# Kernel tuning notes

Measured on AMD Instinct MI355X. Metric: run time of the kernel, lower is better.

The kernel has to match this reference:

```python
import jax, jax.numpy as jnp
import numpy as np

BETA = 0.25


def setup_inputs() -> dict:
    key = jax.random.key(0)
    k1, k2 = jax.random.split(key)
    z = jax.random.normal(k1, (16, 2048, 256), dtype=jnp.float32)
    # n_q=4 codebooks, each [n_e=2048, e_dim=256]; xavier-ish scale
    W = jax.random.normal(k2, (4, 2048, 256), dtype=jnp.float32) * 0.05
    return {"z": z, "W": W}


def reference(z, W):
    """Residual VQ forward (p=1.0, eval-mode math). Returns (z_q, loss, indices)."""
    n_q, n_e, e_dim = W.shape
    lead = z.shape[:-1]
    flat_shape = (-1, e_dim)

    residual = z
    cumulative_q = jnp.zeros_like(z)
    losses = []
    idx_list = []
    for k in range(n_q):
        Wk = W[k]  # [n_e, e_dim]
        flat = residual.reshape(flat_shape)  # [N, e_dim]
        dist = (
            jnp.sum(flat * flat, axis=1, keepdims=True)
            - 2.0 * (flat @ Wk.T)
            + jnp.sum(Wk * Wk, axis=1)[None, :]
        )
        idx = jnp.argmin(dist, axis=1)  # [N]
        # one_hot @ Wk is mathematically a gather of codebook rows
        q = Wk[idx].reshape(residual.shape)
        # commit + beta*codebook; both are (residual.detach() - q)^2.mean(-1)
        diff = jax.lax.stop_gradient(residual) - q
        losses.append((1.0 + BETA) * jnp.mean(diff * diff, axis=-1))
        cumulative_q = cumulative_q + q
        residual = residual - q
        idx_list.append(idx.reshape(*lead, 1))

    # straight-through: gradient of z_q flows only to z
    z_q = z + jax.lax.stop_gradient(cumulative_q - z)
    total_loss = jnp.mean(jnp.stack(losses, axis=0).mean(axis=0))
    indices = jnp.concatenate(idx_list, axis=-1)  # [..., n_q]
    return z_q, total_loss, indices
```

## Files before the change

kernel.cpp:

```cpp
#include <hip/hip_runtime.h>
#include <cstdint>
#include <math.h>
#include <float.h>

#define N_Q   4
#define NROWS 32768
#define EDIM  256
#define NE    2048
#define NCT_H 64
#define TM    32
#define NTHREADS 256

#define ZQ_SIZE  (NROWS * EDIM)
#define LOSS_OFF ZQ_SIZE
#define IDX_OFF  (ZQ_SIZE + 1)

#define TAU 0.012f

typedef __attribute__((ext_vector_type(8))) _Float16 f16x8;
typedef __attribute__((ext_vector_type(4))) float    f32x4;

union F8 { _Float16 h[8]; f16x8 v; };

__device__ __forceinline__ float np_block128_sq(const float* __restrict__ p) {
    #pragma clang fp contract(off)
    float r[8];
    #pragma unroll
    for (int j = 0; j < 8; ++j) { float v = p[j]; r[j] = v * v; }
    for (int i = 8; i < 128; i += 8) {
        #pragma unroll
        for (int j = 0; j < 8; ++j) { float v = p[i + j]; float sq = v * v; r[j] = r[j] + sq; }
    }
    return ((r[0] + r[1]) + (r[2] + r[3])) + ((r[4] + r[5]) + (r[6] + r[7]));
}

__global__ __launch_bounds__(256) void wsq_kernel(const float* __restrict__ W,
                                                  float* __restrict__ wsq32) {
    __shared__ float rowbuf[4][EDIM];
    int wv   = threadIdx.x >> 6;
    int row  = blockIdx.x * 4 + (threadIdx.x >> 6);
    int lane = threadIdx.x & 63;
    float4 v = ((const float4*)(W + (size_t)row * EDIM))[lane];
    *(float4*)&rowbuf[wv][lane * 4] = v;
    __syncthreads();
    if (lane == 0) {
        float a = np_block128_sq(rowbuf[wv]);
        float b = np_block128_sq(rowbuf[wv] + 128);
        wsq32[row] = a + b;
    }
}

__global__ __launch_bounds__(256) void wh_kernel(const float* __restrict__ W,
                                                 short* __restrict__ wh) {
    int gid  = blockIdx.x * 256 + threadIdx.x;
    int lane = gid & 63;
    int grp  = gid >> 6;
    int ctq  = grp >> 3;
    int ks   = grp & 7;
    int n = lane & 15, kq = lane >> 4;
    const float* src = W + (((size_t)(ctq * 16 + n)) << 8) + ks * 32 + kq * 8;
    float4 p0 = *(const float4*)src;
    float4 p1 = *(const float4*)(src + 4);
    float v[8] = {p0.x, p0.y, p0.z, p0.w, p1.x, p1.y, p1.z, p1.w};
    F8 h;
    #pragma unroll
    for (int j = 0; j < 8; ++j) h.h[j] = (_Float16)v[j];
    *(f16x8*)(wh + (((size_t)grp) << 9) + lane * 8) = h.v;
}

__device__ __forceinline__ void top3_merge(float& a1, int& ai1, float& a2, int& ai2, float& a3,
                                           float b1, int bi1, float b2, int bi2, float b3) {
    float c1, c2, c3; int k1, k2;
    if (b1 < a1 || (b1 == a1 && bi1 < ai1)) {
        c1 = b1; k1 = bi1;
        if (a1 < b2 || (a1 == b2 && ai1 < bi2)) { c2 = a1; k2 = ai1; c3 = fminf(b2, a2); }
        else                                    { c2 = b2; k2 = bi2; c3 = fminf(a1, b3); }
    } else {
        c1 = a1; k1 = ai1;
        if (b1 < a2 || (b1 == a2 && bi1 < ai2)) { c2 = b1; k2 = bi1; c3 = fminf(a2, b2); }
        else                                    { c2 = a2; k2 = ai2; c3 = fminf(b1, a3); }
    }
    a1 = c1; ai1 = k1; a2 = c2; ai2 = k2; a3 = c3;
}

__global__ __launch_bounds__(256, 4) void rvq_main(
    const float* __restrict__ z, const float* __restrict__ W,
    const float* __restrict__ wsq32, const short* __restrict__ wh,
    float* __restrict__ resd_g, float* __restrict__ out,
    float* __restrict__ loss_partial)
{
    __shared__ __align__(16) short lds_b[2][2][4][512];
    __shared__ float Srow[TM];
    __shared__ float rm1[2][TM], rm2[2][TM], rm3[2][TM];
    __shared__ int   ri1[2][TM], ri2[2][TM];
    __shared__ int   idx_s[TM], is2_s[TM];
    __shared__ int   rk_cnt, rk_list[TM];
    __shared__ int   pr_cnt, pr_list[TM];
    __shared__ float rrow_s[EDIM];
    __shared__ float red_f[NTHREADS];
    __shared__ int   red_i[NTHREADS];
    __shared__ float wavesum[4];

    const int tid  = threadIdx.x;
    const int wave = tid >> 6;
    const int lane = tid & 63;
    const int n    = lane & 15;
    const int kq   = lane >> 4;
    const int half = wave >> 1;
    const int rsel = wave & 1;
    const int row0 = blockIdx.x * TM;
    const int rowg = row0 + rsel * 16;

    for (int i = tid; i < TM * 64; i += NTHREADS) {
        int r = i >> 6, c = i & 63;
        ((float4*)resd_g)[(((size_t)(row0 + r)) << 6) + c] =
            ((const float4*)z)[(((size_t)(row0 + r)) << 6) + c];
    }

    float lsum = 0.f;

    for (int q = 0; q < N_Q; ++q) {
        const float* Wk   = W + (size_t)q * NE * EDIM;
        const float* wsqk = wsq32 + q * NE;
        const short* whq  = wh + ((size_t)q << 19);

        __syncthreads();
        if (tid == 0) { rk_cnt = 0; pr_cnt = 0; }
        if (tid < 2 * TM) {
            int r = tid >> 1, hf = tid & 1;
            float s = np_block128_sq(resd_g + (((size_t)(row0 + r)) << 8) + hf * 128);
            float s2 = __shfl_xor(s, 1, 64);
            if (hf == 0) Srow[r] = s + s2;
        }
        __syncthreads();

        f16x8 ah[8];
        #pragma unroll
        for (int ks = 0; ks < 8; ++ks) {
            const float* rp = resd_g + (((size_t)(rowg + n)) << 8) + ks * 32 + kq * 8;
            float4 p0 = *(const float4*)rp;
            float4 p1 = *(const float4*)(rp + 4);
            float v[8] = {p0.x, p0.y, p0.z, p0.w, p1.x, p1.y, p1.z, p1.w};
            F8 h;
            #pragma unroll
            for (int j = 0; j < 8; ++j) h.h[j] = (_Float16)v[j];
            ah[ks] = h.v;
        }
        float sreg[4];
        #pragma unroll
        for (int rg = 0; rg < 4; ++rg)
            sreg[rg] = Srow[rsel * 16 + kq * 4 + rg];

        float M1[4], M2[4], M3[4]; int I1[4], I2[4];
        #pragma unroll
        for (int s = 0; s < 4; ++s) {
            M1[s] = INFINITY; M2[s] = INFINITY; M3[s] = INFINITY; I1[s] = 0; I2[s] = 0;
        }

        auto stage = [&](int buf, int ct, int kp) {
            #pragma unroll
            for (int j = 0; j < 2; ++j) {
                int ksl = (wave & 1) * 2 + j;
                size_t grp = ((size_t)((wave >> 1) * 64 + ct) << 3) + kp * 4 + ksl;
                const short* gp = whq + (grp << 9) + lane * 8;
                __builtin_amdgcn_global_load_lds(
                    (const __attribute__((address_space(1))) void*)gp,
                    (__attribute__((address_space(3))) void*)&lds_b[buf][wave >> 1][ksl][0],
                    16, 0, 0);
            }
        };

        f32x4 acc;
        stage(0, 0, 0);
        __syncthreads();

        for (int ct = 0; ct < NCT_H; ++ct) {
            float wq = wsqk[(half * 64 + ct) * 16 + n];

            stage(1, ct, 1);
            acc = (f32x4){0.f, 0.f, 0.f, 0.f};
            #pragma unroll
            for (int ksl = 0; ksl < 4; ++ksl) {
                f16x8 bh = *(const f16x8*)&lds_b[0][half][ksl][lane * 8];
                acc = __builtin_amdgcn_mfma_f32_16x16x32_f16(ah[ksl], bh, acc, 0, 0, 0);
            }
            __syncthreads();

            if (ct + 1 < NCT_H) stage(0, ct + 1, 0);
            #pragma unroll
            for (int ksl = 0; ksl < 4; ++ksl) {
                f16x8 bh = *(const f16x8*)&lds_b[1][half][ksl][lane * 8];
                acc = __builtin_amdgcn_mfma_f32_16x16x32_f16(ah[4 + ksl], bh, acc, 0, 0, 0);
            }

            int cg = (half * 64 + ct) * 16 + n;
            #pragma unroll
            for (int s = 0; s < 4; ++s) {
                float d = fmaf(-2.0f, acc[s], sreg[s]) + wq;
                bool c1 = d < M1[s];
                bool c2 = d < M2[s];
                M3[s] = fminf(M3[s], fmaxf(M2[s], d));
                M2[s] = fminf(M2[s], fmaxf(M1[s], d));
                I2[s] = c1 ? I1[s] : (c2 ? cg : I2[s]);
                M1[s] = fminf(M1[s], d);
                I1[s] = c1 ? cg : I1[s];
            }
            __syncthreads();
        }

        #pragma unroll
        for (int s = 0; s < 4; ++s) {
            float a1 = M1[s], a2 = M2[s], a3 = M3[s]; int ai = I1[s], aj = I2[s];
            #pragma unroll
            for (int mask = 1; mask < 16; mask <<= 1) {
                float b1 = __shfl_xor(a1, mask, 64);
                float b2 = __shfl_xor(a2, mask, 64);
                float b3 = __shfl_xor(a3, mask, 64);
                int   bi = __shfl_xor(ai, mask, 64);
                int   bj = __shfl_xor(aj, mask, 64);
                top3_merge(a1, ai, a2, aj, a3, b1, bi, b2, bj, b3);
            }
            if (n == 0) {
                int rr = rsel * 16 + kq * 4 + s;
                rm1[half][rr] = a1; rm2[half][rr] = a2; rm3[half][rr] = a3;
                ri1[half][rr] = ai; ri2[half][rr] = aj;
            }
        }
        __syncthreads();

        if (tid < TM) {
            float a1 = rm1[0][tid], a2 = rm2[0][tid], a3 = rm3[0][tid];
            int ai = ri1[0][tid], aj = ri2[0][tid];
            top3_merge(a1, ai, a2, aj, a3,
                       rm1[1][tid], ri1[1][tid], rm2[1][tid], ri2[1][tid], rm3[1][tid]);
            idx_s[tid] = ai; is2_s[tid] = aj;
            if (a2 - a1 <= TAU) {
                if (a3 - a1 > TAU) { int p = atomicAdd(&pr_cnt, 1); pr_list[p] = tid; }
                else               { int p = atomicAdd(&rk_cnt, 1); rk_list[p] = tid; }
            }
        }
        __syncthreads();

        {
            int ncheck = rk_cnt;
            for (int f = 0; f < ncheck; ++f) {
                int r = rk_list[f];
                if (tid < 64)
                    ((float4*)rrow_s)[tid] =
                        ((const float4*)(resd_g + (((size_t)(row0 + r)) << 8)))[tid];
                __syncthreads();
                float Sr = Srow[r];
                float accv[8];
                #pragma unroll
                for (int j = 0; j < 8; ++j) accv[j] = 0.f;
                const float* wp = Wk + ((size_t)tid * 8) * EDIM;
                for (int kb = 0; kb < 64; ++kb) {
                    float4 rv = *(const float4*)&rrow_s[kb * 4];
                    #pragma unroll
                    for (int j = 0; j < 8; ++j) {
                        float4 wv = *(const float4*)(wp + j * EDIM + kb * 4);
                        accv[j] = fmaf(rv.x, wv.x, accv[j]);
                        accv[j] = fmaf(rv.y, wv.y, accv[j]);
                        accv[j] = fmaf(rv.z, wv.z, accv[j]);
                        accv[j] = fmaf(rv.w, wv.w, accv[j]);
                    }
                }
                float bm = FLT_MAX; int bi = 0;
                #pragma unroll
                for (int j = 0; j < 8; ++j) {
                    int c = tid * 8 + j;
                    float d = fmaf(-2.0f, accv[j], Sr) + wsqk[c];
                    if (d < bm) { bm = d; bi = c; }
                }
                red_f[tid] = bm; red_i[tid] = bi;
                __syncthreads();
                for (int off = 128; off > 0; off >>= 1) {
                    if (tid < off) {
                        float v = red_f[tid + off]; int ii = red_i[tid + off];
                        if (v < red_f[tid] || (v == red_f[tid] && ii < red_i[tid])) {
                            red_f[tid] = v; red_i[tid] = ii;
                        }
                    }
                    __syncthreads();
                }
                if (tid == 0) idx_s[r] = red_i[0];
                __syncthreads();
            }
        }

        {
            int cnt2 = pr_cnt * 2;
            for (int base = 0; base < cnt2; base += NTHREADS) {
                int slot = base + tid;
                float d = FLT_MAX; int code = 0; int r = -1;
                if (slot < cnt2) {
                    r = pr_list[slot >> 1];
                    code = (slot & 1) ? is2_s[r] : idx_s[r];
                    const float* rp = resd_g + (((size_t)(row0 + r)) << 8);
                    const float* wp = Wk + ((size_t)code << 8);
                    float acc1 = 0.f;
                    for (int kb = 0; kb < 64; ++kb) {
                        float4 rv = *(const float4*)(rp + kb * 4);
                        float4 wv = *(const float4*)(wp + kb * 4);
                        acc1 = fmaf(rv.x, wv.x, acc1);
                        acc1 = fmaf(rv.y, wv.y, acc1);
                        acc1 = fmaf(rv.z, wv.z, acc1);
                        acc1 = fmaf(rv.w, wv.w, acc1);
                    }
                    d = fmaf(-2.0f, acc1, Srow[r]) + wsqk[code];
                }
                float dp = __shfl_xor(d, 1, 64);
                int   cp = __shfl_xor(code, 1, 64);
                if (slot < cnt2 && (slot & 1) == 0) {
                    idx_s[r] = (dp < d || (dp == d && cp < code)) ? cp : code;
                }
            }
        }
        __syncthreads();

        if (tid < TM)
            out[IDX_OFF + (size_t)(row0 + tid) * N_Q + q] = (float)idx_s[tid];
        __syncthreads();

        {
            const int d = tid;
            for (int r = 0; r < TM; ++r) {
                float w = Wk[(((size_t)idx_s[r]) << 8) + d];
                float* rp = resd_g + (((size_t)(row0 + r)) << 8) + d;
                float nv = *rp - w;
                *rp = nv;
                lsum = fmaf(nv, nv, lsum);
            }
        }
    }

    __syncthreads();
    for (int i = tid; i < TM * 64; i += NTHREADS) {
        int r = i >> 6, c = i & 63;
        float4 zv = ((const float4*)z)[(((size_t)(row0 + r)) << 6) + c];
        float4 rv = ((const float4*)resd_g)[(((size_t)(row0 + r)) << 6) + c];
        float4 o = {zv.x - rv.x, zv.y - rv.y, zv.z - rv.z, zv.w - rv.w};
        ((float4*)out)[(((size_t)(row0 + r)) << 6) + c] = o;
    }
    #pragma unroll
    for (int off = 32; off > 0; off >>= 1) lsum += __shfl_down(lsum, off, 64);
    if (lane == 0) wavesum[wave] = lsum;
    __syncthreads();
    if (tid == 0)
        loss_partial[blockIdx.x] = wavesum[0] + wavesum[1] + wavesum[2] + wavesum[3];
}

__global__ __launch_bounds__(256) void loss_reduce(const float* __restrict__ partial,
                                                   float* __restrict__ out) {
    __shared__ float sh[256];
    int t = threadIdx.x;
    sh[t] = partial[t] + partial[t + 256] + partial[t + 512] + partial[t + 768];
    __syncthreads();
    for (int off = 128; off > 0; off >>= 1) {
        if (t < off) sh[t] += sh[t + off];
        __syncthreads();
    }
    if (t == 0)
        out[LOSS_OFF] = sh[0] * (1.25f / ((float)N_Q * (float)NROWS * (float)EDIM));
}

extern "C" void kernel_launch(void* const* d_in, const int* in_sizes, int n_in,
                              void* d_out, int out_size, void* d_ws, size_t ws_size,
                              hipStream_t stream) {
    const float* z = (const float*)d_in[0];
    const float* W = (const float*)d_in[1];
    float* out = (float*)d_out;

    float* wsq32   = (float*)d_ws;
    float* partial = (float*)((char*)d_ws + 32768);
    short* wh      = (short*)((char*)d_ws + 65536);
    float* resd    = (float*)((char*)d_ws + 65536 + 8388608);

    hipLaunchKernelGGL(wsq_kernel, dim3(NE * N_Q / 4), dim3(NTHREADS), 0, stream, W, wsq32);
    hipLaunchKernelGGL(wh_kernel, dim3(1024), dim3(NTHREADS), 0, stream, W, wh);
    hipLaunchKernelGGL(rvq_main, dim3(NROWS / TM), dim3(NTHREADS), 0, stream,
                       z, W, wsq32, wh, resd, out, partial);
    hipLaunchKernelGGL(loss_reduce, dim3(1), dim3(NTHREADS), 0, stream, partial, out);
}
```

Measured before the change: 698.0 us.

## Keep residual rows in registers and double row tile per block

Each thread now keeps its 16x? residual slice in registers (rsd[8][8]) for all four stages, so the global residual scratch buffer and its per-stage reads and writes go away. Each block handles 64 rows with every wave covering all 2048 codes, which doubles reuse of each staged codebook tile and removes the cross-half top-3 merge. Rescoring rows are copied from registers through LDS buffers. The cost is higher register pressure (launch bounds lowered to 2 blocks per CU), half as many blocks, and rescoring batched in groups of 8 rows with extra barriers.

```diff
diff --git a/kernel.cpp b/kernel.cpp
--- a/kernel.cpp
+++ b/kernel.cpp
@@ -7,8 +7,8 @@
 #define NROWS 32768
 #define EDIM  256
 #define NE    2048
-#define NCT_H 64
-#define TM    32
+#define NCT   64
+#define TM    64
 #define NTHREADS 256
 
 #define ZQ_SIZE  (NROWS * EDIM)
@@ -83,20 +83,18 @@
     a1 = c1; ai1 = k1; a2 = c2; ai2 = k2; a3 = c3;
 }
 
-__global__ __launch_bounds__(256, 4) void rvq_main(
+__global__ __launch_bounds__(256, 2) void rvq_main(
     const float* __restrict__ z, const float* __restrict__ W,
     const float* __restrict__ wsq32, const short* __restrict__ wh,
-    float* __restrict__ resd_g, float* __restrict__ out,
-    float* __restrict__ loss_partial)
+    float* __restrict__ out, float* __restrict__ loss_partial)
 {
     __shared__ __align__(16) short lds_b[2][2][4][512];
     __shared__ float Srow[TM];
-    __shared__ float rm1[2][TM], rm2[2][TM], rm3[2][TM];
-    __shared__ int   ri1[2][TM], ri2[2][TM];
     __shared__ int   idx_s[TM], is2_s[TM];
     __shared__ int   rk_cnt, rk_list[TM];
     __shared__ int   pr_cnt, pr_list[TM];
-    __shared__ float rrow_s[EDIM];
+    __shared__ __align__(16) float rrow_s[EDIM];
+    __shared__ __align__(16) float prbuf[8][EDIM];
     __shared__ float red_f[NTHREADS];
     __shared__ int   red_i[NTHREADS];
     __shared__ float wavesum[4];
@@ -106,15 +104,19 @@
     const int lane = tid & 63;
     const int n    = lane & 15;
     const int kq   = lane >> 4;
-    const int half = wave >> 1;
-    const int rsel = wave & 1;
     const int row0 = blockIdx.x * TM;
-    const int rowg = row0 + rsel * 16;
-
-    for (int i = tid; i < TM * 64; i += NTHREADS) {
-        int r = i >> 6, c = i & 63;
-        ((float4*)resd_g)[(((size_t)(row0 + r)) << 6) + c] =
-            ((const float4*)z)[(((size_t)(row0 + r)) << 6) + c];
+    const int myrow = row0 + wave * 16 + n;
+
+    float rsd[8][8];
+    {
+        const float* zp = z + (((size_t)myrow) << 8) + kq * 8;
+        #pragma unroll
+        for (int ks = 0; ks < 8; ++ks) {
+            float4 a = *(const float4*)(zp + ks * 32);
+            float4 b = *(const float4*)(zp + ks * 32 + 4);
+            rsd[ks][0] = a.x; rsd[ks][1] = a.y; rsd[ks][2] = a.z; rsd[ks][3] = a.w;
+            rsd[ks][4] = b.x; rsd[ks][5] = b.y; rsd[ks][6] = b.z; rsd[ks][7] = b.w;
+        }
     }
 
     float lsum = 0.f;
@@ -126,84 +128,103 @@
 
         __syncthreads();
         if (tid == 0) { rk_cnt = 0; pr_cnt = 0; }
-        if (tid < 2 * TM) {
-            int r = tid >> 1, hf = tid & 1;
-            float s = np_block128_sq(resd_g + (((size_t)(row0 + r)) << 8) + hf * 128);
-            float s2 = __shfl_xor(s, 1, 64);
-            if (hf == 0) Srow[r] = s + s2;
-        }
-        __syncthreads();
-
-        f16x8 ah[8];
-        #pragma unroll
-        for (int ks = 0; ks < 8; ++ks) {
-            const float* rp = resd_g + (((size_t)(rowg + n)) << 8) + ks * 32 + kq * 8;
-            float4 p0 = *(const float4*)rp;
-            float4 p1 = *(const float4*)(rp + 4);
-            float v[8] = {p0.x, p0.y, p0.z, p0.w, p1.x, p1.y, p1.z, p1.w};
-            F8 h;
-            #pragma unroll
-            for (int j = 0; j < 8; ++j) h.h[j] = (_Float16)v[j];
-            ah[ks] = h.v;
-        }
-        float sreg[4];
-        #pragma unroll
-        for (int rg = 0; rg < 4; ++rg)
-            sreg[rg] = Srow[rsel * 16 + kq * 4 + rg];
-
-        float M1[4], M2[4], M3[4]; int I1[4], I2[4];
-        #pragma unroll
-        for (int s = 0; s < 4; ++s) {
-            M1[s] = INFINITY; M2[s] = INFINITY; M3[s] = INFINITY; I1[s] = 0; I2[s] = 0;
-        }
 
         auto stage = [&](int buf, int ct, int kp) {
             #pragma unroll
             for (int j = 0; j < 2; ++j) {
-                int ksl = (wave & 1) * 2 + j;
-                size_t grp = ((size_t)((wave >> 1) * 64 + ct) << 3) + kp * 4 + ksl;
+                int c   = wave * 2 + j;
+                int hf  = c >> 2, ksl = c & 3;
+                size_t grp = ((size_t)(hf * 64 + ct) << 3) + kp * 4 + ksl;
                 const short* gp = whq + (grp << 9) + lane * 8;
                 __builtin_amdgcn_global_load_lds(
                     (const __attribute__((address_space(1))) void*)gp,
-                    (__attribute__((address_space(3))) void*)&lds_b[buf][wave >> 1][ksl][0],
+                    (__attribute__((address_space(3))) void*)&lds_b[buf][hf][ksl][0],
                     16, 0, 0);
             }
         };
-
-        f32x4 acc;
         stage(0, 0, 0);
+
+        {
+            float sp = 0.f;
+            #pragma unroll
+            for (int ks = 0; ks < 8; ++ks)
+                #pragma unroll
+                for (int j = 0; j < 8; ++j) sp = fmaf(rsd[ks][j], rsd[ks][j], sp);
+            sp += __shfl_xor(sp, 16, 64);
+            sp += __shfl_xor(sp, 32, 64);
+            if (kq == 0) Srow[wave * 16 + n] = sp;
+        }
+
+        f16x8 ah[8];
+        #pragma unroll
+        for (int ks = 0; ks < 8; ++ks) {
+            F8 h;
+            #pragma unroll
+            for (int j = 0; j < 8; ++j) h.h[j] = (_Float16)rsd[ks][j];
+            ah[ks] = h.v;
+        }
         __syncthreads();
 
-        for (int ct = 0; ct < NCT_H; ++ct) {
-            float wq = wsqk[(half * 64 + ct) * 16 + n];
+        float sreg[4];
+        #pragma unroll
+        for (int rg = 0; rg < 4; ++rg)
+            sreg[rg] = Srow[wave * 16 + kq * 4 + rg];
+
+        float M1[4], M2[4], M3[4]; int I1[4], I2[4];
+        #pragma unroll
+        for (int s = 0; s < 4; ++s) {
+            M1[s] = INFINITY; M2[s] = INFINITY; M3[s] = INFINITY; I1[s] = 0; I2[s] = 0;
+        }
+
+        f32x4 acc0, acc1;
+        for (int ct = 0; ct < NCT; ++ct) {
+            float wq0 = wsqk[ct * 16 + n];
+            float wq1 = wsqk[1024 + ct * 16 + n];
 
             stage(1, ct, 1);
-            acc = (f32x4){0.f, 0.f, 0.f, 0.f};
+            acc0 = (f32x4){0.f, 0.f, 0.f, 0.f};
+            acc1 = (f32x4){0.f, 0.f, 0.f, 0.f};
             #pragma unroll
             for (int ksl = 0; ksl < 4; ++ksl) {
-                f16x8 bh = *(const f16x8*)&lds_b[0][half][ksl][lane * 8];
-                acc = __builtin_amdgcn_mfma_f32_16x16x32_f16(ah[ksl], bh, acc, 0, 0, 0);
+                f16x8 b0 = *(const f16x8*)&lds_b[0][0][ksl][lane * 8];
+                f16x8 b1 = *(const f16x8*)&lds_b[0][1][ksl][lane * 8];
+                acc0 = __builtin_amdgcn_mfma_f32_16x16x32_f16(ah[ksl], b0, acc0, 0, 0, 0);
+                acc1 = __builtin_amdgcn_mfma_f32_16x16x32_f16(ah[ksl], b1, acc1, 0, 0, 0);
             }
             __syncthreads();
 
-            if (ct + 1 < NCT_H) stage(0, ct + 1, 0);
+            if (ct + 1 < NCT) stage(0, ct + 1, 0);
             #pragma unroll
             for (int ksl = 0; ksl < 4; ++ksl) {
-                f16x8 bh = *(const f16x8*)&lds_b[1][half][ksl][lane * 8];
-                acc = __builtin_amdgcn_mfma_f32_16x16x32_f16(ah[4 + ksl], bh, acc, 0, 0, 0);
-            }
-
-            int cg = (half * 64 + ct) * 16 + n;
+                f16x8 b0 = *(const f16x8*)&lds_b[1][0][ksl][lane * 8];
+                f16x8 b1 = *(const f16x8*)&lds_b[1][1][ksl][lane * 8];
+                acc0 = __builtin_amdgcn_mfma_f32_16x16x32_f16(ah[4 + ksl], b0, acc0, 0, 0, 0);
+                acc1 = __builtin_amdgcn_mfma_f32_16x16x32_f16(ah[4 + ksl], b1, acc1, 0, 0, 0);
+            }
+
+            int cg0 = ct * 16 + n;
+            int cg1 = 1024 + ct * 16 + n;
             #pragma unroll
             for (int s = 0; s < 4; ++s) {
-                float d = fmaf(-2.0f, acc[s], sreg[s]) + wq;
+                float d = fmaf(-2.0f, acc0[s], sreg[s]) + wq0;
                 bool c1 = d < M1[s];
                 bool c2 = d < M2[s];
                 M3[s] = fminf(M3[s], fmaxf(M2[s], d));
                 M2[s] = fminf(M2[s], fmaxf(M1[s], d));
-                I2[s] = c1 ? I1[s] : (c2 ? cg : I2[s]);
+                I2[s] = c1 ? I1[s] : (c2 ? cg0 : I2[s]);
                 M1[s] = fminf(M1[s], d);
-                I1[s] = c1 ? cg : I1[s];
+                I1[s] = c1 ? cg0 : I1[s];
+            }
+            #pragma unroll
+            for (int s = 0; s < 4; ++s) {
+                float d = fmaf(-2.0f, acc1[s], sreg[s]) + wq1;
+                bool c1 = d < M1[s];
+                bool c2 = d < M2[s];
+                M3[s] = fminf(M3[s], fmaxf(M2[s], d));
+                M2[s] = fminf(M2[s], fmaxf(M1[s], d));
+                I2[s] = c1 ? I1[s] : (c2 ? cg1 : I2[s]);
+                M1[s] = fminf(M1[s], d);
+                I1[s] = c1 ? cg1 : I1[s];
             }
             __syncthreads();
         }
@@ -221,22 +242,12 @@
                 top3_merge(a1, ai, a2, aj, a3, b1, bi, b2, bj, b3);
             }
             if (n == 0) {
-                int rr = rsel * 16 + kq * 4 + s;
-                rm1[half][rr] = a1; rm2[half][rr] = a2; rm3[half][rr] = a3;
-                ri1[half][rr] = ai; ri2[half][rr] = aj;
-            }
-        }
-        __syncthreads();
-
-        if (tid < TM) {
-            float a1 = rm1[0][tid], a2 = rm2[0][tid], a3 = rm3[0][tid];
-            int ai = ri1[0][tid], aj = ri2[0][tid];
-            top3_merge(a1, ai, a2, aj, a3,
-                       rm1[1][tid], ri1[1][tid], rm2[1][tid], ri2[1][tid], rm3[1][tid]);
-            idx_s[tid] = ai; is2_s[tid] = aj;
-            if (a2 - a1 <= TAU) {
-                if (a3 - a1 > TAU) { int p = atomicAdd(&pr_cnt, 1); pr_list[p] = tid; }
-                else               { int p = atomicAdd(&rk_cnt, 1); rk_list[p] = tid; }
+                int r = wave * 16 + kq * 4 + s;
+                idx_s[r] = ai; is2_s[r] = aj;
+                if (a2 - a1 <= TAU) {
+                    if (a3 - a1 > TAU) { int p = atomicAdd(&pr_cnt, 1); pr_list[p] = r; }
+                    else               { int p = atomicAdd(&rk_cnt, 1); rk_list[p] = r; }
+                }
             }
         }
         __syncthreads();
@@ -245,11 +256,17 @@
             int ncheck = rk_cnt;
             for (int f = 0; f < ncheck; ++f) {
                 int r = rk_list[f];
-                if (tid < 64)
-                    ((float4*)rrow_s)[tid] =
-                        ((const float4*)(resd_g + (((size_t)(row0 + r)) << 8)))[tid];
+                if (wave == (r >> 4) && n == (r & 15)) {
+                    #pragma unroll
+                    for (int ks = 0; ks < 8; ++ks) {
+                        *(float4*)&rrow_s[ks * 32 + kq * 8] =
+                            (float4){rsd[ks][0], rsd[ks][1], rsd[ks][2], rsd[ks][3]};
+                        *(float4*)&rrow_s[ks * 32 + kq * 8 + 4] =
+                            (float4){rsd[ks][4], rsd[ks][5], rsd[ks][6], rsd[ks][7]};
+                    }
+                }
                 __syncthreads();
-                float Sr = Srow[r];
+                float Sr = np_block128_sq(rrow_s) + np_block128_sq(rrow_s + 128);
                 float accv[8];
                 #pragma unroll
                 for (int j = 0; j < 8; ++j) accv[j] = 0.f;
@@ -289,58 +306,85 @@
         }
 
         {
-            int cnt2 = pr_cnt * 2;
-            for (int base = 0; base < cnt2; base += NTHREADS) {
-                int slot = base + tid;
+            int cnt = pr_cnt;
+            for (int base = 0; base < cnt; base += 8) {
+                int bend = (base + 8 < cnt) ? base + 8 : cnt;
+                for (int f = base; f < bend; ++f) {
+                    int r = pr_list[f];
+                    if (wave == (r >> 4) && n == (r & 15)) {
+                        #pragma unroll
+                        for (int ks = 0; ks < 8; ++ks) {
+                            *(float4*)&prbuf[f - base][ks * 32 + kq * 8] =
+                                (float4){rsd[ks][0], rsd[ks][1], rsd[ks][2], rsd[ks][3]};
+                            *(float4*)&prbuf[f - base][ks * 32 + kq * 8 + 4] =
+                                (float4){rsd[ks][4], rsd[ks][5], rsd[ks][6], rsd[ks][7]};
+                        }
+                    }
+                }
+                __syncthreads();
+                int bcnt2 = (bend - base) * 2;
+                int slot = tid;
                 float d = FLT_MAX; int code = 0; int r = -1;
-                if (slot < cnt2) {
-                    r = pr_list[slot >> 1];
+                if (slot < bcnt2) {
+                    r = pr_list[base + (slot >> 1)];
                     code = (slot & 1) ? is2_s[r] : idx_s[r];
-                    const float* rp = resd_g + (((size_t)(row0 + r)) << 8);
+                    const float* rp = prbuf[slot >> 1];
+                    float Sr = np_block128_sq(rp) + np_block128_sq(rp + 128);
                     const float* wp = Wk + ((size_t)code << 8);
-                    float acc1 = 0.f;
+                    float acc1v = 0.f;
                     for (int kb = 0; kb < 64; ++kb) {
                         float4 rv = *(const float4*)(rp + kb * 4);
                         float4 wv = *(const float4*)(wp + kb * 4);
-                        acc1 = fmaf(rv.x, wv.x, acc1);
-                        acc1 = fmaf(rv.y, wv.y, acc1);
-                        acc1 = fmaf(rv.z, wv.z, acc1);
-                        acc1 = fmaf(rv.w, wv.w, acc1);
+                        acc1v = fmaf(rv.x, wv.x, acc1v);
+                        acc1v = fmaf(rv.y, wv.y, acc1v);
+                        acc1v = fmaf(rv.z, wv.z, acc1v);
+                        acc1v = fmaf(rv.w, wv.w, acc1v);
                     }
-                    d = fmaf(-2.0f, acc1, Srow[r]) + wsqk[code];
+                    d = fmaf(-2.0f, acc1v, Sr) + wsqk[code];
                 }
                 float dp = __shfl_xor(d, 1, 64);
                 int   cp = __shfl_xor(code, 1, 64);
-                if (slot < cnt2 && (slot & 1) == 0) {
+                if (slot < bcnt2 && (slot & 1) == 0) {
                     idx_s[r] = (dp < d || (dp == d && cp < code)) ? cp : code;
                 }
+                __syncthreads();
             }
         }
         __syncthreads();
 
         if (tid < TM)
             out[IDX_OFF + (size_t)(row0 + tid) * N_Q + q] = (float)idx_s[tid];
-        __syncthreads();
 
         {
-            const int d = tid;
-            for (int r = 0; r < TM; ++r) {
-                float w = Wk[(((size_t)idx_s[r]) << 8) + d];
-                float* rp = resd_g + (((size_t)(row0 + r)) << 8) + d;
-                float nv = *rp - w;
-                *rp = nv;
-                lsum = fmaf(nv, nv, lsum);
-            }
-        }
-    }
-
-    __syncthreads();
-    for (int i = tid; i < TM * 64; i += NTHREADS) {
-        int r = i >> 6, c = i & 63;
-        float4 zv = ((const float4*)z)[(((size_t)(row0 + r)) << 6) + c];
-        float4 rv = ((const float4*)resd_g)[(((size_t)(row0 + r)) << 6) + c];
-        float4 o = {zv.x - rv.x, zv.y - rv.y, zv.z - rv.z, zv.w - rv.w};
-        ((float4*)out)[(((size_t)(row0 + r)) << 6) + c] = o;
+            int code = idx_s[wave * 16 + n];
+            const float* wp = Wk + (((size_t)code) << 8) + kq * 8;
+            #pragma unroll
+            for (int ks = 0; ks < 8; ++ks) {
+                float4 a = *(const float4*)(wp + ks * 32);
+                float4 b = *(const float4*)(wp + ks * 32 + 4);
+                float w[8] = {a.x, a.y, a.z, a.w, b.x, b.y, b.z, b.w};
+                #pragma unroll
+                for (int j = 0; j < 8; ++j) {
+                    float nv = rsd[ks][j] - w[j];
+                    rsd[ks][j] = nv;
+                    lsum = fmaf(nv, nv, lsum);
+                }
+            }
+        }
+    }
+
+    {
+        const float* zp = z + (((size_t)myrow) << 8) + kq * 8;
+        float* op = out + (((size_t)myrow) << 8) + kq * 8;
+        #pragma unroll
+        for (int ks = 0; ks < 8; ++ks) {
+            float4 a = *(const float4*)(zp + ks * 32);
+            float4 b = *(const float4*)(zp + ks * 32 + 4);
+            float4 o0 = {a.x - rsd[ks][0], a.y - rsd[ks][1], a.z - rsd[ks][2], a.w - rsd[ks][3]};
+            float4 o1 = {b.x - rsd[ks][4], b.y - rsd[ks][5], b.z - rsd[ks][6], b.w - rsd[ks][7]};
+            *(float4*)(op + ks * 32)     = o0;
+            *(float4*)(op + ks * 32 + 4) = o1;
+        }
     }
     #pragma unroll
     for (int off = 32; off > 0; off >>= 1) lsum += __shfl_down(lsum, off, 64);
@@ -354,7 +398,7 @@
                                                    float* __restrict__ out) {
     __shared__ float sh[256];
     int t = threadIdx.x;
-    sh[t] = partial[t] + partial[t + 256] + partial[t + 512] + partial[t + 768];
+    sh[t] = partial[t] + partial[t + 256];
     __syncthreads();
     for (int off = 128; off > 0; off >>= 1) {
         if (t < off) sh[t] += sh[t + off];
@@ -374,11 +418,10 @@
     float* wsq32   = (float*)d_ws;
     float* partial = (float*)((char*)d_ws + 32768);
     short* wh      = (short*)((char*)d_ws + 65536);
-    float* resd    = (float*)((char*)d_ws + 65536 + 8388608);
 
     hipLaunchKernelGGL(wsq_kernel, dim3(NE * N_Q / 4), dim3(NTHREADS), 0, stream, W, wsq32);
     hipLaunchKernelGGL(wh_kernel, dim3(1024), dim3(NTHREADS), 0, stream, W, wh);
     hipLaunchKernelGGL(rvq_main, dim3(NROWS / TM), dim3(NTHREADS), 0, stream,
-                       z, W, wsq32, wh, resd, out, partial);
+                       z, W, wsq32, wh, out, partial);
     hipLaunchKernelGGL(loss_reduce, dim3(1), dim3(NTHREADS), 0, stream, partial, out);
 }
```

New measurement: 754.3 us. 1.08x slower.
